# Performance work log

Hardware: AMD Instinct MI355X
Metric: run time of the kernel (lower is better)

Reference implementation:

```python
import jax, jax.numpy as jnp
import numpy as np

N_NODES = 100000
N_EDGES = 1600000
VOCAB = 1000
EMB = 128
HID = 256
N_GRAPHS = 128
N_LABELS = 2


def setup_inputs() -> dict:
    key = jax.random.key(0)
    ks = jax.random.split(key, 16)
    s = 0.05
    inp = {
        "x_ids": jax.random.randint(ks[0], (N_NODES,), 0, VOCAB),
        "edge_index": jax.random.randint(ks[1], (2, N_EDGES), 0, N_NODES),
        "batch": jnp.sort(jax.random.randint(ks[2], (N_NODES,), 0, N_GRAPHS)),
        "emb": jax.random.normal(ks[3], (VOCAB, EMB)) * s,
        "W0": jax.random.normal(ks[4], (EMB, HID)) * s,
        "b0": jnp.zeros((HID,)),
        "W1": jax.random.normal(ks[5], (HID, HID)) * s,
        "b1": jnp.zeros((HID,)),
        "W2": jax.random.normal(ks[6], (HID, HID)) * s,
        "b2": jnp.zeros((HID,)),
        "W3": jax.random.normal(ks[7], (HID, HID)) * s,
        "b3": jnp.zeros((HID,)),
        "Wc1": jax.random.normal(ks[8], (2 * HID, HID)) * s,
        "bc1": jnp.zeros((HID,)),
        "Wc2": jax.random.normal(ks[9], (HID, N_LABELS)) * s,
        "bc2": jnp.zeros((N_LABELS,)),
    }
    return inp


def _gcn_conv(x, W, b, src, dst, dis):
    # GCNConv with self-loops: out = D^-1/2 (A+I) D^-1/2 (x W) + b
    xw = x @ W                                   # [N, H]
    norm = dis[src] * dis[dst]                   # [E]
    out = jnp.zeros_like(xw).at[dst].add(xw[src] * norm[:, None])
    out = out + xw * (dis * dis)[:, None]        # self-loop term
    return out + b


def reference(x_ids, edge_index, batch, emb, W0, b0, W1, b1, W2, b2, W3, b3,
              Wc1, bc1, Wc2, bc2):
    src, dst = edge_index[0], edge_index[1]
    # degree (incl. self loop) is the same every layer -> compute once
    deg = jnp.zeros((N_NODES,), jnp.float32).at[dst].add(1.0) + 1.0
    dis = jax.lax.rsqrt(deg)

    x = emb[x_ids]                               # [N, EMB]
    for W, b in ((W0, b0), (W1, b1), (W2, b2), (W3, b3)):
        x = jax.nn.relu(_gcn_conv(x, W, b, src, dst, dis))
        # dropout: identity in eval mode

    counts = jax.ops.segment_sum(jnp.ones((N_NODES,), x.dtype), batch,
                                 num_segments=N_GRAPHS)
    mean_pool = jax.ops.segment_sum(x, batch, num_segments=N_GRAPHS)
    mean_pool = mean_pool / jnp.maximum(counts, 1.0)[:, None]
    max_pool = jax.ops.segment_max(x, batch, num_segments=N_GRAPHS)
    max_pool = jnp.where(counts[:, None] > 0, max_pool, 0.0)

    g = jnp.concatenate([mean_pool, max_pool], axis=1)  # [G, 2H]
    h = jax.nn.relu(g @ Wc1 + bc1)
    logits = h @ Wc2 + bc2                               # [G, 2]
    return logits
```

## Files before the change

kernel.cpp:

```cpp
#include <hip/hip_runtime.h>
#include <hip/hip_bf16.h>
#include <cstdint>
#include <cstddef>

#define N_NODES 100000
#define N_EDGES 1600000
#define EMBD 128
#define HID 256
#define N_GRAPHS 128
#define VOCAB 1000
#define NB_SCAN 98

typedef short bf16x8 __attribute__((ext_vector_type(8)));
typedef float f32x4 __attribute__((ext_vector_type(4)));
typedef float f32x2 __attribute__((ext_vector_type(2)));

__device__ inline unsigned short rne_bf16(float f) {
  unsigned u = __float_as_uint(f);
  return (unsigned short)((u + 0x7FFFu + ((u >> 16) & 1u)) >> 16);
}
__device__ inline float bf16_to_f32(unsigned short h) {
  return __uint_as_float(((unsigned)h) << 16);
}
__device__ inline void split_hl(float v, unsigned short& h, unsigned short& l) {
  h = rne_bf16(v);
  float hf = __uint_as_float(((unsigned)h) << 16);
  l = rne_bf16(v - hf);
}
__device__ inline f32x4 cvt4(uint2 v) {
  f32x4 r;
  r[0] = __uint_as_float(v.x << 16);
  r[1] = __uint_as_float(v.x & 0xFFFF0000u);
  r[2] = __uint_as_float(v.y << 16);
  r[3] = __uint_as_float(v.y & 0xFFFF0000u);
  return r;
}
__device__ inline f32x2 cvt2(unsigned v) {
  f32x2 r;
  r[0] = __uint_as_float(v << 16);
  r[1] = __uint_as_float(v & 0xFFFF0000u);
  return r;
}

__global__ void k_indeg(const int* __restrict__ dst, int* __restrict__ indeg) {
  int e = blockIdx.x * 256 + threadIdx.x;
  if (e < N_EDGES) atomicAdd(&indeg[dst[e]], 1);
}

__global__ __launch_bounds__(1024)
void k_scan1(const int* __restrict__ indeg, int* __restrict__ off, int* __restrict__ bsum,
             float* __restrict__ dis) {
  __shared__ int s[1024];
  const int tid = threadIdx.x;
  int i = blockIdx.x * 1024 + tid;
  int v = (i < N_NODES) ? indeg[i] : 0;
  if (i < N_NODES) dis[i] = rsqrtf((float)(v + 1));
  s[tid] = v; __syncthreads();
  #pragma unroll
  for (int ofs = 1; ofs < 1024; ofs <<= 1) {
    int t2 = (tid >= ofs) ? s[tid - ofs] : 0;
    __syncthreads();
    s[tid] += t2;
    __syncthreads();
  }
  if (i < N_NODES) off[i] = s[tid] - v;
  if (tid == 1023) bsum[blockIdx.x] = s[1023];
}

__global__ void k_scan2(int* __restrict__ bsum) {
  if (threadIdx.x == 0) {
    int a = 0;
    for (int i = 0; i < NB_SCAN; ++i) { int t = bsum[i]; bsum[i] = a; a += t; }
    bsum[NB_SCAN] = a;
  }
}

__global__ __launch_bounds__(1024)
void k_scan3(int* __restrict__ off, int* __restrict__ cur, const int* __restrict__ bsum) {
  int i = blockIdx.x * 1024 + threadIdx.x;
  if (i < N_NODES) { int v = off[i] + bsum[blockIdx.x]; off[i] = v; cur[i] = v; }
  if (i == 0) off[N_NODES] = bsum[NB_SCAN];
}

__global__ void k_fill(const int* __restrict__ src, const int* __restrict__ dst,
                       const int* __restrict__ ids, const float* __restrict__ dis,
                       int* __restrict__ cursor, int2* __restrict__ csre,
                       int2* __restrict__ csre0) {
  int e = blockIdx.x * 256 + threadIdx.x;
  if (e < N_EDGES) {
    int s = src[e];
    float ds = dis[s];
    int p = atomicAdd(&cursor[dst[e]], 1);
    csre[p]  = make_int2(s, __float_as_int(ds));
    csre0[p] = make_int2(ids[s], __float_as_int(ds));
  }
}

__global__ void k_prep(const float* __restrict__ emb, unsigned short* __restrict__ emb16,
                       const float* __restrict__ W0, unsigned short* __restrict__ w0h,
                       unsigned short* __restrict__ w0l,
                       const float* __restrict__ W1, unsigned short* __restrict__ w1h,
                       unsigned short* __restrict__ w1l,
                       const float* __restrict__ W2, unsigned short* __restrict__ w2h,
                       unsigned short* __restrict__ w2l,
                       const float* __restrict__ W3, unsigned short* __restrict__ w3h,
                       unsigned short* __restrict__ w3l) {
  int i = blockIdx.x * 256 + threadIdx.x;
  if (i < VOCAB * EMBD) { emb16[i] = rne_bf16(emb[i]); return; }
  i -= VOCAB * EMBD;
  unsigned short h, l;
  if (i < EMBD * HID) {
    int k = i >> 8, n = i & 255;
    split_hl(W0[i], h, l);
    w0h[n * EMBD + k] = h; w0l[n * EMBD + k] = l;
    return;
  }
  i -= EMBD * HID;
  if (i >= 3 * HID * HID) return;
  int w = i >> 16, j = i & 65535;
  const float* Ws = (w == 0) ? W1 : (w == 1) ? W2 : W3;
  unsigned short* th = (w == 0) ? w1h : (w == 1) ? w2h : w3h;
  unsigned short* tl = (w == 0) ? w1l : (w == 1) ? w2l : w3l;
  int k = j >> 8, n = j & 255;
  split_hl(Ws[j], h, l);
  th[n * HID + k] = h; tl[n * HID + k] = l;
}

__global__ __launch_bounds__(256)
void k_agg0(const unsigned short* __restrict__ emb16, const int* __restrict__ ids,
            const float* __restrict__ dis, const int* __restrict__ off,
            const int2* __restrict__ csre0, unsigned short* __restrict__ aggA) {
  const int lane = threadIdx.x & 63;
  const int node = blockIdx.x * 4 + (threadIdx.x >> 6);
  const float di = dis[node];
  unsigned sv = *((const unsigned*)(emb16 + (size_t)ids[node] * EMBD) + lane);
  f32x2 a0 = di * cvt2(sv);
  f32x2 a1 = (f32x2)0.f, a2 = (f32x2)0.f, a3 = (f32x2)0.f;
  const int e0 = off[node], e1 = off[node + 1];
  int e = e0;
  for (; e + 4 <= e1; e += 4) {
    int2 c0 = csre0[e], c1 = csre0[e + 1], c2 = csre0[e + 2], c3 = csre0[e + 3];
    unsigned v0 = *((const unsigned*)(emb16 + (size_t)c0.x * EMBD) + lane);
    unsigned v1 = *((const unsigned*)(emb16 + (size_t)c1.x * EMBD) + lane);
    unsigned v2 = *((const unsigned*)(emb16 + (size_t)c2.x * EMBD) + lane);
    unsigned v3 = *((const unsigned*)(emb16 + (size_t)c3.x * EMBD) + lane);
    a0 += __int_as_float(c0.y) * cvt2(v0);
    a1 += __int_as_float(c1.y) * cvt2(v1);
    a2 += __int_as_float(c2.y) * cvt2(v2);
    a3 += __int_as_float(c3.y) * cvt2(v3);
  }
  for (; e < e1; ++e) {
    int2 c0 = csre0[e];
    unsigned v0 = *((const unsigned*)(emb16 + (size_t)c0.x * EMBD) + lane);
    a0 += __int_as_float(c0.y) * cvt2(v0);
  }
  f32x2 r = di * ((a0 + a1) + (a2 + a3));
  size_t base = (size_t)node * EMBD + lane * 2;
  *(ushort2*)&aggA[base] = make_ushort2(rne_bf16(r[0]), rne_bf16(r[1]));
}

__global__ __launch_bounds__(256)
void k_agg16(const unsigned short* __restrict__ y16, const float* __restrict__ dis,
             const int* __restrict__ off, const int2* __restrict__ csre,
             unsigned short* __restrict__ aggA) {
  const int lane = threadIdx.x & 63;
  const int node = blockIdx.x * 4 + (threadIdx.x >> 6);
  const float di = dis[node];
  uint2 sv = *((const uint2*)(y16 + (size_t)node * HID) + lane);
  f32x4 a0 = di * cvt4(sv);
  f32x4 a1 = (f32x4)0.f, a2 = (f32x4)0.f, a3 = (f32x4)0.f;
  const int e0 = off[node], e1 = off[node + 1];
  int e = e0;
  for (; e + 8 <= e1; e += 8) {
    int2 c0 = csre[e],     c1 = csre[e + 1], c2 = csre[e + 2], c3 = csre[e + 3];
    int2 c4 = csre[e + 4], c5 = csre[e + 5], c6 = csre[e + 6], c7 = csre[e + 7];
    uint2 v0 = *((const uint2*)(y16 + (size_t)c0.x * HID) + lane);
    uint2 v1 = *((const uint2*)(y16 + (size_t)c1.x * HID) + lane);
    uint2 v2 = *((const uint2*)(y16 + (size_t)c2.x * HID) + lane);
    uint2 v3 = *((const uint2*)(y16 + (size_t)c3.x * HID) + lane);
    uint2 v4 = *((const uint2*)(y16 + (size_t)c4.x * HID) + lane);
    uint2 v5 = *((const uint2*)(y16 + (size_t)c5.x * HID) + lane);
    uint2 v6 = *((const uint2*)(y16 + (size_t)c6.x * HID) + lane);
    uint2 v7 = *((const uint2*)(y16 + (size_t)c7.x * HID) + lane);
    a0 += __int_as_float(c0.y) * cvt4(v0);
    a1 += __int_as_float(c1.y) * cvt4(v1);
    a2 += __int_as_float(c2.y) * cvt4(v2);
    a3 += __int_as_float(c3.y) * cvt4(v3);
    a0 += __int_as_float(c4.y) * cvt4(v4);
    a1 += __int_as_float(c5.y) * cvt4(v5);
    a2 += __int_as_float(c6.y) * cvt4(v6);
    a3 += __int_as_float(c7.y) * cvt4(v7);
  }
  for (; e + 4 <= e1; e += 4) {
    int2 c0 = csre[e], c1 = csre[e + 1], c2 = csre[e + 2], c3 = csre[e + 3];
    uint2 v0 = *((const uint2*)(y16 + (size_t)c0.x * HID) + lane);
    uint2 v1 = *((const uint2*)(y16 + (size_t)c1.x * HID) + lane);
    uint2 v2 = *((const uint2*)(y16 + (size_t)c2.x * HID) + lane);
    uint2 v3 = *((const uint2*)(y16 + (size_t)c3.x * HID) + lane);
    a0 += __int_as_float(c0.y) * cvt4(v0);
    a1 += __int_as_float(c1.y) * cvt4(v1);
    a2 += __int_as_float(c2.y) * cvt4(v2);
    a3 += __int_as_float(c3.y) * cvt4(v3);
  }
  for (; e < e1; ++e) {
    int2 c0 = csre[e];
    uint2 v0 = *((const uint2*)(y16 + (size_t)c0.x * HID) + lane);
    a0 += __int_as_float(c0.y) * cvt4(v0);
  }
  f32x4 r = di * ((a0 + a1) + (a2 + a3));
  size_t base = (size_t)node * HID + lane * 4;
  *(ushort4*)&aggA[base] = make_ushort4(rne_bf16(r[0]), rne_bf16(r[1]),
                                        rne_bf16(r[2]), rne_bf16(r[3]));
}

__device__ inline void gl_lds16(const void* g, void* l) {
  __builtin_amdgcn_global_load_lds((const __attribute__((address_space(1))) unsigned int*)g,
                                   (__attribute__((address_space(3))) unsigned int*)l,
                                   16, 0, 0);
}

template<int K>
__global__ __launch_bounds__(256)
void k_gemm_mfma(const unsigned short* __restrict__ Ah,
                 const unsigned short* __restrict__ Wh, const unsigned short* __restrict__ Wl,
                 const float* __restrict__ bias, unsigned short* __restrict__ C16) {
  __shared__ unsigned short sA[2][128 * 32];
  __shared__ unsigned short sBh[2][128 * 32];
  __shared__ unsigned short sBl[2][128 * 32];
  const int tid = threadIdx.x;
  const int lane = tid & 63;
  const int wid = tid >> 6;
  const int wr = wid >> 1, wc = wid & 1;
  const int row0 = blockIdx.x * 128;
  const int col0 = blockIdx.y * 128;
  const int cl = lane & 15;
  const int sl = lane >> 4;
  const int nt = K / 32;

  f32x4 acc[4][4];
  #pragma unroll
  for (int i = 0; i < 4; ++i)
    #pragma unroll
    for (int j = 0; j < 4; ++j) acc[i][j] = (f32x4)0.f;

  auto stage = [&](int b, int kt) {
    #pragma unroll
    for (int q = 0; q < 2; ++q) {
      int c = (wid * 2 + q) * 64 + lane;
      int row = c >> 2, slot = c & 3;
      int ss = slot ^ (row & 3);
      int ga = row0 + row; if (ga > N_NODES - 1) ga = N_NODES - 1;
      size_t aoff = (size_t)ga * K + kt + ss * 8;
      gl_lds16(Ah + aoff, &sA[b][(wid * 2 + q) * 512]);
      size_t boff = (size_t)(col0 + row) * K + kt + ss * 8;
      gl_lds16(Wh + boff, &sBh[b][(wid * 2 + q) * 512]);
      gl_lds16(Wl + boff, &sBl[b][(wid * 2 + q) * 512]);
    }
  };

  stage(0, 0);
  __syncthreads();

  for (int t = 0; t < nt; ++t) {
    const int cur = t & 1;
    if (t + 1 < nt) stage(cur ^ 1, (t + 1) * 32);

    bf16x8 fa[4], fbh[4], fbl[4];
    #pragma unroll
    for (int f = 0; f < 4; ++f) {
      int ra = wr * 64 + f * 16 + cl;
      int oa = ra * 32 + ((sl ^ (ra & 3)) << 3);
      fa[f] = *(const bf16x8*)&sA[cur][oa];
      int rb = wc * 64 + f * 16 + cl;
      int ob = rb * 32 + ((sl ^ (rb & 3)) << 3);
      fbh[f] = *(const bf16x8*)&sBh[cur][ob];
      fbl[f] = *(const bf16x8*)&sBl[cur][ob];
    }
    #pragma unroll
    for (int i = 0; i < 4; ++i)
      #pragma unroll
      for (int j = 0; j < 4; ++j) {
        acc[i][j] = __builtin_amdgcn_mfma_f32_16x16x32_bf16(fa[i], fbh[j], acc[i][j], 0, 0, 0);
        acc[i][j] = __builtin_amdgcn_mfma_f32_16x16x32_bf16(fa[i], fbl[j], acc[i][j], 0, 0, 0);
      }
    __syncthreads();
  }

  #pragma unroll
  for (int j = 0; j < 4; ++j) {
    int gn = col0 + wc * 64 + j * 16 + cl;
    float bn = bias[gn];
    #pragma unroll
    for (int i = 0; i < 4; ++i) {
      f32x4 v = acc[i][j];
      #pragma unroll
      for (int r = 0; r < 4; ++r) {
        int gm = row0 + wr * 64 + i * 16 + sl * 4 + r;
        if (gm < N_NODES) C16[(size_t)gm * HID + gn] = rne_bf16(fmaxf(v[r] + bn, 0.f));
      }
    }
  }
}

__device__ inline int lower_bound_i(const int* a, int n, int v) {
  int lo = 0, hi = n;
  while (lo < hi) { int m = (lo + hi) >> 1; if (a[m] < v) lo = m + 1; else hi = m; }
  return lo;
}

__global__ __launch_bounds__(256)
void k_pool(const unsigned short* __restrict__ y16, const int* __restrict__ batch,
            float* __restrict__ gsum, float* __restrict__ gmax) {
  const int gi = blockIdx.x, ck = blockIdx.y, t = threadIdx.x;
  const int start = lower_bound_i(batch, N_NODES, gi);
  const int end   = lower_bound_i(batch, N_NODES, gi + 1);
  const int len = end - start;
  const int c0 = start + (len * ck) / 4;
  const int c1 = start + (len * (ck + 1)) / 4;
  float sum = 0.f, mx = 0.f;
  #pragma unroll 4
  for (int n = c0; n < c1; ++n) {
    float v = bf16_to_f32(y16[(size_t)n * HID + t]);
    sum += v; mx = fmaxf(mx, v);
  }
  if (c0 < c1) {
    atomicAdd(&gsum[gi * HID + t], sum);
    atomicMax((int*)&gmax[gi * HID + t], __float_as_int(mx));
  }
}

__global__ __launch_bounds__(256)
void k_cls(const float* __restrict__ gsum, const float* __restrict__ gmax,
           const int* __restrict__ batch,
           const float* __restrict__ Wc1, const float* __restrict__ bc1,
           const float* __restrict__ Wc2, const float* __restrict__ bc2,
           float* __restrict__ out) {
  const int gi = blockIdx.x, t = threadIdx.x;
  __shared__ float sg[512];
  __shared__ float sh[256];
  const int start = lower_bound_i(batch, N_NODES, gi);
  const int end   = lower_bound_i(batch, N_NODES, gi + 1);
  const float rcnt = 1.f / (float)((end - start) > 0 ? (end - start) : 1);
  sg[t] = gsum[gi * HID + t] * rcnt;
  sg[256 + t] = gmax[gi * HID + t];
  __syncthreads();
  float a = bc1[t];
  #pragma unroll 8
  for (int k = 0; k < 512; ++k) a = fmaf(sg[k], Wc1[k * HID + t], a);
  sh[t] = fmaxf(a, 0.f);
  __syncthreads();
  if (t < 2) {
    float o = bc2[t];
    for (int k = 0; k < 256; ++k) o = fmaf(sh[k], Wc2[k * 2 + t], o);
    out[gi * 2 + t] = o;
  }
}

extern "C" void kernel_launch(void* const* d_in, const int* in_sizes, int n_in,
                              void* d_out, int out_size, void* d_ws, size_t ws_size,
                              hipStream_t stream) {
  const int*   x_ids = (const int*)d_in[0];
  const int*   ei    = (const int*)d_in[1];
  const int*   batch = (const int*)d_in[2];
  const float* emb   = (const float*)d_in[3];
  const float* W0 = (const float*)d_in[4];  const float* b0 = (const float*)d_in[5];
  const float* W1 = (const float*)d_in[6];  const float* b1 = (const float*)d_in[7];
  const float* W2 = (const float*)d_in[8];  const float* b2 = (const float*)d_in[9];
  const float* W3 = (const float*)d_in[10]; const float* b3 = (const float*)d_in[11];
  const float* Wc1 = (const float*)d_in[12]; const float* bc1 = (const float*)d_in[13];
  const float* Wc2 = (const float*)d_in[14]; const float* bc2 = (const float*)d_in[15];
  float* out = (float*)d_out;
  const int* src = ei;
  const int* dst = ei + N_EDGES;

  char* ws = (char*)d_ws;
  size_t o = 0;
  auto alloc = [&](size_t bytes) -> char* {
    char* p = ws + o; o += (bytes + 255) & ~(size_t)255; return p;
  };
  unsigned short* y16  = (unsigned short*)alloc((size_t)N_NODES * HID * 2);
  unsigned short* aggA = (unsigned short*)alloc((size_t)N_NODES * HID * 2);
  float* dis   = (float*)alloc((size_t)N_NODES * 4);
  int*   indeg = (int*)  alloc((size_t)N_NODES * 4);
  int*   off   = (int*)  alloc((size_t)(N_NODES + 1) * 4);
  int*   cur   = (int*)  alloc((size_t)(N_NODES + 1) * 4);
  int*   bsum  = (int*)  alloc((size_t)(NB_SCAN + 1) * 4);
  int2*  csre  = (int2*) alloc((size_t)N_EDGES * 8);
  int2*  csre0 = (int2*) alloc((size_t)N_EDGES * 8);
  unsigned short* emb16 = (unsigned short*)alloc((size_t)VOCAB * EMBD * 2);
  unsigned short* wbuf  = (unsigned short*)alloc((size_t)458752 * 2);
  float* gsum  = (float*)alloc((size_t)N_GRAPHS * HID * 4);
  float* gmax  = (float*)alloc((size_t)N_GRAPHS * HID * 4);
  (void)ws_size; (void)in_sizes; (void)n_in; (void)out_size;

  unsigned short* wt0h = wbuf;            unsigned short* wt0l = wbuf + 32768;
  unsigned short* wt1h = wbuf + 65536;    unsigned short* wt1l = wbuf + 131072;
  unsigned short* wt2h = wbuf + 196608;   unsigned short* wt2l = wbuf + 262144;
  unsigned short* wt3h = wbuf + 327680;   unsigned short* wt3l = wbuf + 393216;

  hipMemsetAsync(indeg, 0, (size_t)N_NODES * 4, stream);
  hipMemsetAsync(gsum, 0, (size_t)N_GRAPHS * HID * 4 * 2 + 256, stream);
  k_indeg<<<N_EDGES / 256, 256, 0, stream>>>(dst, indeg);
  k_scan1<<<NB_SCAN, 1024, 0, stream>>>(indeg, off, bsum, dis);
  k_scan2<<<1, 64, 0, stream>>>(bsum);
  k_scan3<<<NB_SCAN, 1024, 0, stream>>>(off, cur, bsum);
  k_fill<<<N_EDGES / 256, 256, 0, stream>>>(src, dst, x_ids, dis, cur, csre, csre0);
  k_prep<<<(VOCAB * EMBD + EMBD * HID + 3 * HID * HID + 255) / 256, 256, 0, stream>>>(
      emb, emb16, W0, wt0h, wt0l, W1, wt1h, wt1l, W2, wt2h, wt2l, W3, wt3h, wt3l);

  dim3 ggrid((N_NODES + 127) / 128, 2);
  k_agg0<<<N_NODES / 4, 256, 0, stream>>>(emb16, x_ids, dis, off, csre0, aggA);
  k_gemm_mfma<128><<<ggrid, 256, 0, stream>>>(aggA, wt0h, wt0l, b0, y16);
  k_agg16<<<N_NODES / 4, 256, 0, stream>>>(y16, dis, off, csre, aggA);
  k_gemm_mfma<256><<<ggrid, 256, 0, stream>>>(aggA, wt1h, wt1l, b1, y16);
  k_agg16<<<N_NODES / 4, 256, 0, stream>>>(y16, dis, off, csre, aggA);
  k_gemm_mfma<256><<<ggrid, 256, 0, stream>>>(aggA, wt2h, wt2l, b2, y16);
  k_agg16<<<N_NODES / 4, 256, 0, stream>>>(y16, dis, off, csre, aggA);
  k_gemm_mfma<256><<<ggrid, 256, 0, stream>>>(aggA, wt3h, wt3l, b3, y16);

  dim3 pgrid(N_GRAPHS, 4);
  k_pool<<<pgrid, 256, 0, stream>>>(y16, batch, gsum, gmax);
  k_cls<<<N_GRAPHS, 256, 0, stream>>>(gsum, gmax, batch, Wc1, bc1, Wc2, bc2, out);
}
```

Before: 950.6 us.

## Load GEMM fragments directly from global memory and drop aggregation 8-way unroll

The MFMA GEMM no longer stages A and split-bf16 W tiles through double-buffered LDS via global_load_lds; each wave loads its bf16x8 fragments straight from global memory, which removes shared memory and barriers. The 8-edge unrolled loop in the hidden-layer aggregation is removed, so fewer gathers are in flight per wave, and the pooling memset shrinks by 256 bytes. Loading directly loses the LDS sharing of fragments across waves, so the same W and A data is fetched several times through cache, and the aggregation has less memory-level parallelism.

New measurement: 1.079 ms. 1.14x slower.

```diff
diff --git a/kernel.cpp b/kernel.cpp
--- a/kernel.cpp
+++ b/kernel.cpp
@@ -171,26 +171,6 @@
   f32x4 a1 = (f32x4)0.f, a2 = (f32x4)0.f, a3 = (f32x4)0.f;
   const int e0 = off[node], e1 = off[node + 1];
   int e = e0;
-  for (; e + 8 <= e1; e += 8) {
-    int2 c0 = csre[e],     c1 = csre[e + 1], c2 = csre[e + 2], c3 = csre[e + 3];
-    int2 c4 = csre[e + 4], c5 = csre[e + 5], c6 = csre[e + 6], c7 = csre[e + 7];
-    uint2 v0 = *((const uint2*)(y16 + (size_t)c0.x * HID) + lane);
-    uint2 v1 = *((const uint2*)(y16 + (size_t)c1.x * HID) + lane);
-    uint2 v2 = *((const uint2*)(y16 + (size_t)c2.x * HID) + lane);
-    uint2 v3 = *((const uint2*)(y16 + (size_t)c3.x * HID) + lane);
-    uint2 v4 = *((const uint2*)(y16 + (size_t)c4.x * HID) + lane);
-    uint2 v5 = *((const uint2*)(y16 + (size_t)c5.x * HID) + lane);
-    uint2 v6 = *((const uint2*)(y16 + (size_t)c6.x * HID) + lane);
-    uint2 v7 = *((const uint2*)(y16 + (size_t)c7.x * HID) + lane);
-    a0 += __int_as_float(c0.y) * cvt4(v0);
-    a1 += __int_as_float(c1.y) * cvt4(v1);
-    a2 += __int_as_float(c2.y) * cvt4(v2);
-    a3 += __int_as_float(c3.y) * cvt4(v3);
-    a0 += __int_as_float(c4.y) * cvt4(v4);
-    a1 += __int_as_float(c5.y) * cvt4(v5);
-    a2 += __int_as_float(c6.y) * cvt4(v6);
-    a3 += __int_as_float(c7.y) * cvt4(v7);
-  }
   for (; e + 4 <= e1; e += 4) {
     int2 c0 = csre[e], c1 = csre[e + 1], c2 = csre[e + 2], c3 = csre[e + 3];
     uint2 v0 = *((const uint2*)(y16 + (size_t)c0.x * HID) + lane);
@@ -213,29 +193,26 @@
                                         rne_bf16(r[2]), rne_bf16(r[3]));
 }
 
-__device__ inline void gl_lds16(const void* g, void* l) {
-  __builtin_amdgcn_global_load_lds((const __attribute__((address_space(1))) unsigned int*)g,
-                                   (__attribute__((address_space(3))) unsigned int*)l,
-                                   16, 0, 0);
-}
-
 template<int K>
 __global__ __launch_bounds__(256)
-void k_gemm_mfma(const unsigned short* __restrict__ Ah,
-                 const unsigned short* __restrict__ Wh, const unsigned short* __restrict__ Wl,
-                 const float* __restrict__ bias, unsigned short* __restrict__ C16) {
-  __shared__ unsigned short sA[2][128 * 32];
-  __shared__ unsigned short sBh[2][128 * 32];
-  __shared__ unsigned short sBl[2][128 * 32];
-  const int tid = threadIdx.x;
-  const int lane = tid & 63;
-  const int wid = tid >> 6;
+void k_gemm_direct(const unsigned short* __restrict__ A,
+                   const unsigned short* __restrict__ Wh, const unsigned short* __restrict__ Wl,
+                   const float* __restrict__ bias, unsigned short* __restrict__ C16) {
+  const int lane = threadIdx.x & 63;
+  const int wid = threadIdx.x >> 6;
   const int wr = wid >> 1, wc = wid & 1;
   const int row0 = blockIdx.x * 128;
   const int col0 = blockIdx.y * 128;
   const int cl = lane & 15;
   const int sl = lane >> 4;
-  const int nt = K / 32;
+
+  int ra[4];
+  #pragma unroll
+  for (int f = 0; f < 4; ++f) {
+    int r = row0 + wr * 64 + f * 16 + cl;
+    ra[f] = (r < N_NODES) ? r : (N_NODES - 1);
+  }
+  const int cb = col0 + wc * 64 + cl;
 
   f32x4 acc[4][4];
   #pragma unroll
@@ -243,38 +220,14 @@
     #pragma unroll
     for (int j = 0; j < 4; ++j) acc[i][j] = (f32x4)0.f;
 
-  auto stage = [&](int b, int kt) {
-    #pragma unroll
-    for (int q = 0; q < 2; ++q) {
-      int c = (wid * 2 + q) * 64 + lane;
-      int row = c >> 2, slot = c & 3;
-      int ss = slot ^ (row & 3);
-      int ga = row0 + row; if (ga > N_NODES - 1) ga = N_NODES - 1;
-      size_t aoff = (size_t)ga * K + kt + ss * 8;
-      gl_lds16(Ah + aoff, &sA[b][(wid * 2 + q) * 512]);
-      size_t boff = (size_t)(col0 + row) * K + kt + ss * 8;
-      gl_lds16(Wh + boff, &sBh[b][(wid * 2 + q) * 512]);
-      gl_lds16(Wl + boff, &sBl[b][(wid * 2 + q) * 512]);
-    }
-  };
-
-  stage(0, 0);
-  __syncthreads();
-
-  for (int t = 0; t < nt; ++t) {
-    const int cur = t & 1;
-    if (t + 1 < nt) stage(cur ^ 1, (t + 1) * 32);
-
+  #pragma unroll
+  for (int kt = 0; kt < K; kt += 32) {
     bf16x8 fa[4], fbh[4], fbl[4];
     #pragma unroll
     for (int f = 0; f < 4; ++f) {
-      int ra = wr * 64 + f * 16 + cl;
-      int oa = ra * 32 + ((sl ^ (ra & 3)) << 3);
-      fa[f] = *(const bf16x8*)&sA[cur][oa];
-      int rb = wc * 64 + f * 16 + cl;
-      int ob = rb * 32 + ((sl ^ (rb & 3)) << 3);
-      fbh[f] = *(const bf16x8*)&sBh[cur][ob];
-      fbl[f] = *(const bf16x8*)&sBl[cur][ob];
+      fa[f]  = *(const bf16x8*)&A [(size_t)ra[f] * K + kt + sl * 8];
+      fbh[f] = *(const bf16x8*)&Wh[(size_t)(cb + f * 16) * K + kt + sl * 8];
+      fbl[f] = *(const bf16x8*)&Wl[(size_t)(cb + f * 16) * K + kt + sl * 8];
     }
     #pragma unroll
     for (int i = 0; i < 4; ++i)
@@ -283,7 +236,6 @@
         acc[i][j] = __builtin_amdgcn_mfma_f32_16x16x32_bf16(fa[i], fbh[j], acc[i][j], 0, 0, 0);
         acc[i][j] = __builtin_amdgcn_mfma_f32_16x16x32_bf16(fa[i], fbl[j], acc[i][j], 0, 0, 0);
       }
-    __syncthreads();
   }
 
   #pragma unroll
@@ -399,7 +351,7 @@
   unsigned short* wt3h = wbuf + 327680;   unsigned short* wt3l = wbuf + 393216;
 
   hipMemsetAsync(indeg, 0, (size_t)N_NODES * 4, stream);
-  hipMemsetAsync(gsum, 0, (size_t)N_GRAPHS * HID * 4 * 2 + 256, stream);
+  hipMemsetAsync(gsum, 0, (size_t)N_GRAPHS * HID * 4 * 2, stream);
   k_indeg<<<N_EDGES / 256, 256, 0, stream>>>(dst, indeg);
   k_scan1<<<NB_SCAN, 1024, 0, stream>>>(indeg, off, bsum, dis);
   k_scan2<<<1, 64, 0, stream>>>(bsum);
@@ -410,13 +362,13 @@
 
   dim3 ggrid((N_NODES + 127) / 128, 2);
   k_agg0<<<N_NODES / 4, 256, 0, stream>>>(emb16, x_ids, dis, off, csre0, aggA);
-  k_gemm_mfma<128><<<ggrid, 256, 0, stream>>>(aggA, wt0h, wt0l, b0, y16);
+  k_gemm_direct<128><<<ggrid, 256, 0, stream>>>(aggA, wt0h, wt0l, b0, y16);
   k_agg16<<<N_NODES / 4, 256, 0, stream>>>(y16, dis, off, csre, aggA);
-  k_gemm_mfma<256><<<ggrid, 256, 0, stream>>>(aggA, wt1h, wt1l, b1, y16);
+  k_gemm_direct<256><<<ggrid, 256, 0, stream>>>(aggA, wt1h, wt1l, b1, y16);
   k_agg16<<<N_NODES / 4, 256, 0, stream>>>(y16, dis, off, csre, aggA);
-  k_gemm_mfma<256><<<ggrid, 256, 0, stream>>>(aggA, wt2h, wt2l, b2, y16);
+  k_gemm_direct<256><<<ggrid, 256, 0, stream>>>(aggA, wt2h, wt2l, b2, y16);
   k_agg16<<<N_NODES / 4, 256, 0, stream>>>(y16, dis, off, csre, aggA);
-  k_gemm_mfma<256><<<ggrid, 256, 0, stream>>>(aggA, wt3h, wt3l, b3, y16);
+  k_gemm_direct<256><<<ggrid, 256, 0, stream>>>(aggA, wt3h, wt3l, b3, y16);
 
   dim3 pgrid(N_GRAPHS, 4);
   k_pool<<<pgrid, 256, 0, stream>>>(y16, batch, gsum, gmax);
```
